# Optimization experiments

Measured on AMD Instinct MI355X. Metric: run time of the kernel, lower is better.

## Reference

```python
import jax, jax.numpy as jnp
import numpy as np

N_ATOMS = 100000
N_PAIRS = 6400000
NBATCH = 16
RC = 3.0
SIGMA = 1.0
EPSILON = 1.0


def setup_inputs() -> dict:
    key = jax.random.key(0)
    k1, k2, k3 = jax.random.split(key, 3)
    # distances in a physical range (0.8, 3.0), strictly positive, below cutoff rc
    dist = jax.random.uniform(k1, (N_PAIRS,), dtype=jnp.float32, minval=0.8, maxval=RC)
    ind_1 = jax.random.randint(k2, (N_ATOMS, 1), 0, NBATCH, dtype=jnp.int64)
    ind_2 = jax.random.randint(k3, (N_PAIRS, 2), 0, N_ATOMS, dtype=jnp.int64)
    return {"dist": dist, "ind_1": ind_1, "ind_2": ind_2}


def reference(dist, ind_1, ind_2):
    rc, sigma, epsilon = RC, SIGMA, EPSILON
    # energy shift so the potential is zero at the cutoff radius
    e0 = 4.0 * epsilon * ((sigma / rc) ** 12 - (sigma / rc) ** 6)
    c6 = (sigma / dist) ** 6          # [n_pairs]
    c12 = c6 * c6
    en = 4.0 * epsilon * (c12 - c6) - e0
    natom = ind_1.shape[0]            # static
    # scatter per-pair energy onto first atom of each pair
    en_atom = jax.ops.segment_sum(en, ind_2[:, 0], num_segments=natom)
    return en_atom / 2.0
```

## Files before the change

kernel.cpp:

```cpp
#include <hip/hip_runtime.h>


#define CHUNK 8192
#define T1 512
#define ABITS 9
#define APB 512
#define NBMAX 255
#define QSCALE 32768.0f
#define QINV (1.0f / 32768.0f)
#define S_SLICES 8

static __device__ __forceinline__ float half_en(float d) {
    const float half_e0 = -2.739720872119788e-3f;
    float inv = 1.0f / d;
    float i2 = inv * inv;
    float i6 = i2 * i2 * i2;
    return 2.0f * (i6 * i6 - i6) - half_e0;
}

static __device__ __forceinline__ int quant(float e) {
    int q = __float2int_rn(e * QSCALE);
    return max(-4194304, min(4194303, q));
}

__global__ __launch_bounds__(T1) void lj_bin(const float* __restrict__ dist,
                                             const int* __restrict__ ind2,
                                             unsigned* __restrict__ grec,
                                             unsigned* __restrict__ goffs,
                                             int n_pairs, int nblk, int nb) {
    __shared__ unsigned cnt[256];
    __shared__ unsigned offs[256];
    __shared__ unsigned wsum[4];
    __shared__ unsigned recs[CHUNK];

    const int t = threadIdx.x;
    const int c = blockIdx.x;
    const int base = c * CHUNK;

    if (t < 256) cnt[t] = 0;
    __syncthreads();

    unsigned rec[16];
    unsigned br[16];

    #pragma unroll
    for (int g = 0; g < 4; ++g) {
        const int p0 = base + g * (T1 * 4) + t * 4;
        float dd[4] = {0.f, 0.f, 0.f, 0.f};
        int ii[4] = {0, 0, 0, 0};
        if (p0 + 4 <= n_pairs) {
            float4 d = *reinterpret_cast<const float4*>(dist + p0);
            int4 ia = *reinterpret_cast<const int4*>(ind2 + 2 * p0);
            int4 ib = *reinterpret_cast<const int4*>(ind2 + 2 * p0 + 4);
            dd[0] = d.x; dd[1] = d.y; dd[2] = d.z; dd[3] = d.w;
            ii[0] = ia.x; ii[1] = ia.z; ii[2] = ib.x; ii[3] = ib.z;
        } else {
            #pragma unroll
            for (int k = 0; k < 4; ++k)
                if (p0 + k < n_pairs) { dd[k] = dist[p0 + k]; ii[k] = ind2[2 * (p0 + k)]; }
        }
        #pragma unroll
        for (int k = 0; k < 4; ++k) {
            const int j = g * 4 + k;
            if (p0 + k < n_pairs) {
                const int id = ii[k];
                const int b = id >> ABITS;
                const int q = quant(half_en(dd[k]));
                rec[j] = (((unsigned)q) << ABITS) | (unsigned)(id & (APB - 1));
                const unsigned rank = atomicAdd(&cnt[b], 1u);
                br[j] = ((unsigned)b << 16) | rank;
            } else {
                br[j] = 0xFFFFFFFFu;
                rec[j] = 0;
            }
        }
    }
    __syncthreads();

    {
        const unsigned v = (t < 256) ? cnt[t] : 0u;
        unsigned inc = v;
        #pragma unroll
        for (int d = 1; d < 64; d <<= 1) {
            const unsigned x = __shfl_up(inc, d, 64);
            if ((t & 63) >= d) inc += x;
        }
        if (t < 256 && (t & 63) == 63) wsum[t >> 6] = inc;
        __syncthreads();
        if (t < 256) {
            unsigned add = 0;
            #pragma unroll
            for (int j = 0; j < 4; ++j)
                if (j < (t >> 6)) add += wsum[j];
            offs[t] = add + inc - v;
        }
    }
    __syncthreads();

    #pragma unroll
    for (int j = 0; j < 16; ++j) {
        if (br[j] != 0xFFFFFFFFu) {
            const unsigned pos = offs[br[j] >> 16] + (br[j] & 0xFFFFu);
            recs[pos] = rec[j];
        }
    }
    __syncthreads();

    const int nv = min(CHUNK, n_pairs - base);
    for (int i4 = t * 4; i4 + 4 <= nv; i4 += T1 * 4) {
        uint4 v = *reinterpret_cast<const uint4*>(&recs[i4]);
        *reinterpret_cast<uint4*>(&grec[(size_t)base + i4]) = v;
    }
    for (int i = (nv & ~3) + t; i < nv; i += T1)
        grec[(size_t)base + i] = recs[i];
    if (t <= nb)
        goffs[(size_t)t * nblk + c] = offs[t];
}

#define T2 256

__global__ __launch_bounds__(T2) void lj_bucket_reduce(const unsigned* __restrict__ grec,
                                                       const unsigned* __restrict__ goffs,
                                                       int* __restrict__ partial,
                                                       int nblk, int nb, int natom_pad,
                                                       int cps) {
    __shared__ int acc[APB];
    extern __shared__ unsigned dynoffs[];

    const int t = threadIdx.x;
    const int b = blockIdx.x % nb;
    const int s = blockIdx.x / nb;

    #pragma unroll
    for (int k = 0; k < APB / T2; ++k) acc[t + k * T2] = 0;

    const int c0 = s * cps;
    const int cn = min(nblk - c0, cps);
    if (cn <= 0) {
        __syncthreads();
        int* dst = partial + (size_t)s * natom_pad + (size_t)b * APB;
        #pragma unroll
        for (int k = 0; k < APB / T2; ++k) dst[t + k * T2] = acc[t + k * T2];
        return;
    }

    unsigned* lo = dynoffs;
    unsigned* hi = dynoffs + cps;
    const unsigned* r0 = goffs + (size_t)b * nblk + c0;
    const unsigned* r1 = goffs + (size_t)(b + 1) * nblk + c0;
    for (int i = t; i < cn; i += T2) {
        lo[i] = r0[i];
        hi[i] = r1[i];
    }
    __syncthreads();

    const int wv = t >> 6;
    const int ln = t & 63;

    for (int c = wv; c < cn; c += T2 / 64) {
        const unsigned o0 = lo[c];
        const unsigned o1 = hi[c];
        const size_t rb = (size_t)(c0 + c) * CHUNK;
        for (unsigned i = o0 + ln; i < o1; i += 64) {
            const unsigned r = grec[rb + i];
            atomicAdd(&acc[r & (APB - 1)], ((int)r) >> ABITS);
        }
    }
    __syncthreads();

    int* dst = partial + (size_t)s * natom_pad + (size_t)b * APB;
    #pragma unroll
    for (int k = 0; k < APB / T2; ++k) dst[t + k * T2] = acc[t + k * T2];
}

__global__ void lj_final(const int* __restrict__ partial, float* __restrict__ out,
                         int natom, int natom_pad) {
    const int a = blockIdx.x * blockDim.x + threadIdx.x;
    if (a >= natom) return;
    int ssum = 0;
    #pragma unroll
    for (int s = 0; s < S_SLICES; ++s)
        ssum += partial[(size_t)s * natom_pad + a];
    out[a] = (float)ssum * QINV;
}

__global__ void lj_scatter_direct(const float* __restrict__ dist,
                                  const int* __restrict__ ind2,
                                  float* __restrict__ out,
                                  int n_pairs) {
    int t = blockIdx.x * blockDim.x + threadIdx.x;
    int i = t * 4;
    if (i >= n_pairs) return;
    if (i + 4 <= n_pairs) {
        float4 d = *reinterpret_cast<const float4*>(dist + i);
        int4 ia = *reinterpret_cast<const int4*>(ind2 + 2 * i);
        int4 ib = *reinterpret_cast<const int4*>(ind2 + 2 * i + 4);
        atomicAdd(&out[ia.x], half_en(d.x));
        atomicAdd(&out[ia.z], half_en(d.y));
        atomicAdd(&out[ib.x], half_en(d.z));
        atomicAdd(&out[ib.z], half_en(d.w));
    } else {
        for (int p = i; p < n_pairs; ++p)
            atomicAdd(&out[ind2[2 * p]], half_en(dist[p]));
    }
}

extern "C" void kernel_launch(void* const* d_in, const int* in_sizes, int n_in,
                              void* d_out, int out_size, void* d_ws, size_t ws_size,
                              hipStream_t stream) {
    const float* dist = (const float*)d_in[0];
    const int* ind2 = (const int*)d_in[2];
    float* out = (float*)d_out;

    const int n_pairs = in_sizes[0];
    const int natom = out_size;

    const int nblk = (n_pairs + CHUNK - 1) / CHUNK;
    const int nb = (natom + APB - 1) / APB;
    const int natom_pad = nb * APB;
    const int cps = (nblk + S_SLICES - 1) / S_SLICES;

    const size_t rec_bytes = (size_t)nblk * CHUNK * sizeof(unsigned);
    const size_t offs_bytes = (size_t)(nb + 1) * nblk * sizeof(unsigned);
    const size_t part_bytes = (size_t)S_SLICES * natom_pad * sizeof(int);
    const size_t need = rec_bytes + offs_bytes + part_bytes;
    const size_t dyn_lds = 2u * (size_t)cps * sizeof(unsigned);

    if (nb + 1 > 256 || need > ws_size || dyn_lds > 64 * 1024) {
        hipMemsetAsync(d_out, 0, (size_t)out_size * sizeof(float), stream);
        int n_threads = (n_pairs + 3) / 4;
        int grid = (n_threads + 255) / 256;
        lj_scatter_direct<<<grid, 256, 0, stream>>>(dist, ind2, out, n_pairs);
        return;
    }

    unsigned* grec = (unsigned*)d_ws;
    unsigned* goffs = (unsigned*)((char*)d_ws + rec_bytes);
    int* partial = (int*)((char*)d_ws + rec_bytes + offs_bytes);

    lj_bin<<<nblk, T1, 0, stream>>>(dist, ind2, grec, goffs, n_pairs, nblk, nb);
    lj_bucket_reduce<<<S_SLICES * nb, T2, dyn_lds, stream>>>(grec, goffs, partial,
                                                             nblk, nb, natom_pad, cps);
    int fgrid = (natom + 255) / 256;
    lj_final<<<fgrid, 256, 0, stream>>>(partial, out, natom, natom_pad);
}
```

Measured before the change: 43.21 us.

## Interleave chunk-to-slice assignment and split waves into half-wave runs in bucket reduce

```diff
diff --git a/kernel.cpp b/kernel.cpp
--- a/kernel.cpp
+++ b/kernel.cpp
@@ -5,10 +5,10 @@
 #define T1 512
 #define ABITS 9
 #define APB 512
-#define NBMAX 255
 #define QSCALE 32768.0f
 #define QINV (1.0f / 32768.0f)
-#define S_SLICES 8
+#define NS 8
+#define MAXCPS 160
 
 static __device__ __forceinline__ float half_en(float d) {
     const float half_e0 = -2.739720872119788e-3f;
@@ -27,10 +27,10 @@
                                              const int* __restrict__ ind2,
                                              unsigned* __restrict__ grec,
                                              unsigned* __restrict__ goffs,
-                                             int n_pairs, int nblk, int nb) {
+                                             int n_pairs, int nchunk, int nb, int P) {
     __shared__ unsigned cnt[256];
     __shared__ unsigned offs[256];
-    __shared__ unsigned wsum[4];
+    __shared__ unsigned wsum[8];
     __shared__ unsigned recs[CHUNK];
 
     const int t = threadIdx.x;
@@ -114,7 +114,7 @@
     for (int i = (nv & ~3) + t; i < nv; i += T1)
         grec[(size_t)base + i] = recs[i];
     if (t <= nb)
-        goffs[(size_t)t * nblk + c] = offs[t];
+        goffs[((size_t)t * NS + (c & (NS - 1))) * P + (c >> 3)] = offs[t];
 }
 
 #define T2 256
@@ -122,48 +122,43 @@
 __global__ __launch_bounds__(T2) void lj_bucket_reduce(const unsigned* __restrict__ grec,
                                                        const unsigned* __restrict__ goffs,
                                                        int* __restrict__ partial,
-                                                       int nblk, int nb, int natom_pad,
-                                                       int cps) {
+                                                       int nchunk, int nb, int natom_pad,
+                                                       int P) {
     __shared__ int acc[APB];
-    extern __shared__ unsigned dynoffs[];
+    __shared__ unsigned lo[MAXCPS];
+    __shared__ unsigned hi[MAXCPS];
 
     const int t = threadIdx.x;
-    const int b = blockIdx.x % nb;
-    const int s = blockIdx.x / nb;
+    const int vb = blockIdx.x;
+    const int s = vb & (NS - 1);
+    const int b = vb >> 3;
 
     #pragma unroll
     for (int k = 0; k < APB / T2; ++k) acc[t + k * T2] = 0;
 
-    const int c0 = s * cps;
-    const int cn = min(nblk - c0, cps);
-    if (cn <= 0) {
-        __syncthreads();
-        int* dst = partial + (size_t)s * natom_pad + (size_t)b * APB;
-        #pragma unroll
-        for (int k = 0; k < APB / T2; ++k) dst[t + k * T2] = acc[t + k * T2];
-        return;
-    }
-
-    unsigned* lo = dynoffs;
-    unsigned* hi = dynoffs + cps;
-    const unsigned* r0 = goffs + (size_t)b * nblk + c0;
-    const unsigned* r1 = goffs + (size_t)(b + 1) * nblk + c0;
-    for (int i = t; i < cn; i += T2) {
-        lo[i] = r0[i];
-        hi[i] = r1[i];
-    }
-    __syncthreads();
-
-    const int wv = t >> 6;
-    const int ln = t & 63;
-
-    for (int c = wv; c < cn; c += T2 / 64) {
-        const unsigned o0 = lo[c];
-        const unsigned o1 = hi[c];
-        const size_t rb = (size_t)(c0 + c) * CHUNK;
-        for (unsigned i = o0 + ln; i < o1; i += 64) {
-            const unsigned r = grec[rb + i];
-            atomicAdd(&acc[r & (APB - 1)], ((int)r) >> ABITS);
+    const int cn = (nchunk - s + NS - 1) >> 3;
+    if (cn > 0) {
+        const unsigned* r0 = goffs + ((size_t)b * NS + s) * P;
+        const unsigned* r1 = goffs + ((size_t)(b + 1) * NS + s) * P;
+        for (int i = t; i < cn; i += T2) { lo[i] = r0[i]; hi[i] = r1[i]; }
+    }
+    __syncthreads();
+
+    if (cn > 0) {
+        const int wv = t >> 6;
+        const int half = (t >> 5) & 1;
+        const int sub = t & 31;
+        for (int cc = wv * 2; cc < cn; cc += (T2 / 64) * 2) {
+            const int myrun = cc + half;
+            if (myrun < cn) {
+                const unsigned o0 = lo[myrun];
+                const unsigned o1 = hi[myrun];
+                const size_t rb = (size_t)(s + myrun * NS) * CHUNK;
+                for (unsigned i = o0 + sub; i < o1; i += 32) {
+                    const unsigned r = grec[rb + i];
+                    atomicAdd(&acc[r & (APB - 1)], ((int)r) >> ABITS);
+                }
+            }
         }
     }
     __syncthreads();
@@ -179,7 +174,7 @@
     if (a >= natom) return;
     int ssum = 0;
     #pragma unroll
-    for (int s = 0; s < S_SLICES; ++s)
+    for (int s = 0; s < NS; ++s)
         ssum += partial[(size_t)s * natom_pad + a];
     out[a] = (float)ssum * QINV;
 }
@@ -215,18 +210,17 @@
     const int n_pairs = in_sizes[0];
     const int natom = out_size;
 
-    const int nblk = (n_pairs + CHUNK - 1) / CHUNK;
+    const int nchunk = (n_pairs + CHUNK - 1) / CHUNK;
     const int nb = (natom + APB - 1) / APB;
     const int natom_pad = nb * APB;
-    const int cps = (nblk + S_SLICES - 1) / S_SLICES;
-
-    const size_t rec_bytes = (size_t)nblk * CHUNK * sizeof(unsigned);
-    const size_t offs_bytes = (size_t)(nb + 1) * nblk * sizeof(unsigned);
-    const size_t part_bytes = (size_t)S_SLICES * natom_pad * sizeof(int);
+    const int P = (nchunk + NS - 1) / NS;
+
+    const size_t rec_bytes = (size_t)nchunk * CHUNK * sizeof(unsigned);
+    const size_t offs_bytes = (size_t)(nb + 1) * NS * P * sizeof(unsigned);
+    const size_t part_bytes = (size_t)NS * natom_pad * sizeof(int);
     const size_t need = rec_bytes + offs_bytes + part_bytes;
-    const size_t dyn_lds = 2u * (size_t)cps * sizeof(unsigned);
-
-    if (nb + 1 > 256 || need > ws_size || dyn_lds > 64 * 1024) {
+
+    if (nb + 1 > 256 || P > MAXCPS || need > ws_size) {
         hipMemsetAsync(d_out, 0, (size_t)out_size * sizeof(float), stream);
         int n_threads = (n_pairs + 3) / 4;
         int grid = (n_threads + 255) / 256;
@@ -238,9 +232,9 @@
     unsigned* goffs = (unsigned*)((char*)d_ws + rec_bytes);
     int* partial = (int*)((char*)d_ws + rec_bytes + offs_bytes);
 
-    lj_bin<<<nblk, T1, 0, stream>>>(dist, ind2, grec, goffs, n_pairs, nblk, nb);
-    lj_bucket_reduce<<<S_SLICES * nb, T2, dyn_lds, stream>>>(grec, goffs, partial,
-                                                             nblk, nb, natom_pad, cps);
+    lj_bin<<<nchunk, T1, 0, stream>>>(dist, ind2, grec, goffs, n_pairs, nchunk, nb, P);
+    lj_bucket_reduce<<<NS * nb, T2, 0, stream>>>(grec, goffs, partial,
+                                                 nchunk, nb, natom_pad, P);
     int fgrid = (natom + 255) / 256;
     lj_final<<<fgrid, 256, 0, stream>>>(partial, out, natom, natom_pad);
 }
```

Result: faster. 40.30 us (-6.8%).
